# Kernel optimization log

Measured on AMD Instinct MI355X. Metric: run time of the kernel, lower is better.

The kernel has to match this reference:

```python
import jax, jax.numpy as jnp
import numpy as np

N_EXPERTS = 64
TOP_K = 4
D_MODEL = 512
D_FF = 2048
B, T = 2, 1024


def setup_inputs() -> dict:
    key = jax.random.key(0)
    k1, k2, k3, k4 = jax.random.split(key, 4)
    x = jax.random.normal(k1, (B, T, D_MODEL), dtype=jnp.float32)
    hex_weights = jax.random.uniform(k2, (B, T, N_EXPERTS), dtype=jnp.float32)
    W_in = jax.random.normal(k3, (N_EXPERTS, D_FF, D_MODEL), dtype=jnp.float32) * (D_MODEL ** -0.5)
    W_out = jax.random.normal(k4, (N_EXPERTS, D_MODEL, D_FF), dtype=jnp.float32) * (D_FF ** -0.5)
    bias_in = jnp.zeros((N_EXPERTS, D_FF), dtype=jnp.float32)
    bias_out = jnp.zeros((N_EXPERTS, D_MODEL), dtype=jnp.float32)
    return {"x": x, "hex_weights": hex_weights, "W_in": W_in, "bias_in": bias_in,
            "W_out": W_out, "bias_out": bias_out}


def reference(x, hex_weights, W_in, bias_in, W_out, bias_out):
    # x: (B,T,D); hex_weights: (B,T,64)
    Bv, Tv, D = x.shape
    N = Bv * Tv
    xf = x.reshape(N, D)
    hw = hex_weights.reshape(N, N_EXPERTS)
    top_w, top_idx = jax.lax.top_k(hw, TOP_K)                 # (N,K)
    top_w = top_w / (jnp.sum(top_w, axis=-1, keepdims=True) + 1e-8)
    # Sparse combine matrix: row n has top_w at selected experts, 0 elsewhere.
    combine = jnp.zeros((N, N_EXPERTS), dtype=x.dtype).at[
        jnp.arange(N)[:, None], top_idx].add(top_w)            # (N,64)
    # Scan over the 64 experts; equivalent math to per-token weight gather,
    # since combine is zero for unselected experts.
    def body(acc, ew):
        Wi, bi, Wo, bo, c = ew                                 # Wi:(d_ff,D), c:(N,)
        h = jax.nn.silu(xf @ Wi.T + bi)                        # (N,d_ff)
        o = h @ Wo.T + bo                                      # (N,D)
        return acc + c[:, None] * o, None
    out, _ = jax.lax.scan(body, jnp.zeros_like(xf),
                          (W_in, bias_in, W_out, bias_out, combine.T))
    return out.reshape(Bv, Tv, D)
```

## Files before the change

kernel.cpp:

```cpp
#include <hip/hip_runtime.h>
#include <hip/hip_bf16.h>
#include <stdint.h>

#define NTOK 2048
#define NE 64
#define TOPK 4
#define DM 512
#define DF 2048
#define TOTSLOT (NTOK*TOPK)

#define BM 192
#define BK 64
#define GEMM_GRID 1024

typedef __bf16 bf16;
typedef __bf16 bf16x8 __attribute__((ext_vector_type(8)));
typedef __bf16 bf16x4 __attribute__((ext_vector_type(4)));
typedef float  f32x4  __attribute__((ext_vector_type(4)));
typedef short  short8 __attribute__((ext_vector_type(8)));


__global__ void k_route(const float* __restrict__ hw, float* __restrict__ top_w,
                        int* __restrict__ top_idx) {
  int t = blockIdx.x * blockDim.x + threadIdx.x;
  if (t >= NTOK) return;
  const float* r = hw + (size_t)t * NE;
  float rv[NE];
  #pragma unroll
  for (int e = 0; e < NE; ++e) rv[e] = r[e];
  float v[TOPK]; int id[TOPK];
  #pragma unroll
  for (int k = 0; k < TOPK; ++k) {
    float best = -1e30f; int bi = 0;
    #pragma unroll
    for (int e = 0; e < NE; ++e) {
      bool used = false;
      #pragma unroll
      for (int j = 0; j < k; ++j) used |= (id[j] == e);
      if (!used && rv[e] > best) { best = rv[e]; bi = e; }
    }
    v[k] = best; id[k] = bi;
  }
  float den = v[0] + v[1] + v[2] + v[3] + 1e-8f;
  #pragma unroll
  for (int k = 0; k < TOPK; ++k) {
    top_w[t*TOPK + k] = v[k] / den;
    top_idx[t*TOPK + k] = id[k];
  }
}

__global__ __launch_bounds__(256) void k_build(
    const int* __restrict__ top_idx, int* __restrict__ tok,
    int* __restrict__ slot_of, int* __restrict__ offsets_g,
    int* __restrict__ tasklist, int* __restrict__ ntask_g) {
  __shared__ int cnt_s[NE], off_s[NE + 1], fill_s[NE], tpre_s[NE + 1];
  const int tid = threadIdx.x;
  if (tid < NE) { cnt_s[tid] = 0; fill_s[tid] = 0; }
  __syncthreads();
  int ids[TOTSLOT / 256];
  #pragma unroll
  for (int c = 0; c < TOTSLOT / 256; ++c) {
    ids[c] = top_idx[c * 256 + tid];
    atomicAdd(&cnt_s[ids[c]], 1);
  }
  __syncthreads();
  if (tid < 64) {
    int c = cnt_s[tid];
    int inc = c;
    #pragma unroll
    for (int d = 1; d < 64; d <<= 1) {
      int n = __shfl_up(inc, d, 64);
      if (tid >= d) inc += n;
    }
    off_s[tid] = inc - c;
    if (tid == 63) off_s[64] = inc;

    int tc = (c + BM - 1) / BM;
    int tinc = tc;
    #pragma unroll
    for (int d = 1; d < 64; d <<= 1) {
      int n = __shfl_up(tinc, d, 64);
      if (tid >= d) tinc += n;
    }
    tpre_s[tid] = tinc - tc;
    if (tid == 63) tpre_s[64] = tinc;
  }
  __syncthreads();
  #pragma unroll
  for (int c = 0; c < TOTSLOT / 256; ++c) {
    int idx = c * 256 + tid;
    int e = ids[c];
    int pos = off_s[e] + atomicAdd(&fill_s[e], 1);
    tok[pos] = idx >> 2;
    slot_of[idx] = pos;
  }
  if (tid < 64) {
    int tc = (cnt_s[tid] + BM - 1) / BM;
    int base = tpre_s[tid];
    for (int m = 0; m < tc; ++m) tasklist[base + m] = (tid << 8) | m;
    if (tid == 0) *ntask_g = tpre_s[64];
  }
  if (tid <= NE) offsets_g[tid] = off_s[tid];
}

__global__ void k_xcast(const float* __restrict__ x, bf16* __restrict__ xb) {
  int i = blockIdx.x * blockDim.x + threadIdx.x;
  int base = i * 4;
  if (base >= NTOK * DM) return;
  float4 f = *(const float4*)(x + base);
  bf16x4 o;
  o[0] = (bf16)f.x; o[1] = (bf16)f.y; o[2] = (bf16)f.z; o[3] = (bf16)f.w;
  *(bf16x4*)(xb + base) = o;
}


template<int PASS, int BNT>
__global__ __launch_bounds__(512) void k_gemm(
    const float* __restrict__ W, const float* __restrict__ bias,
    const bf16* __restrict__ Asrc, const int* __restrict__ tok,
    const int* __restrict__ offsets,
    const int* __restrict__ tasklist, const int* __restrict__ ntask_g,
    bf16* __restrict__ Hout, float* __restrict__ Oout)
{
  constexpr int KFULL = (PASS == 1) ? DM : DF;
  constexpr int KT    = KFULL / BK;
  constexpr int NDIM  = (PASS == 1) ? DF : DM;
  constexpr int NT    = NDIM / BNT;
  constexpr int TPR   = 512 / BNT;
  constexpr int NQ    = 16 / TPR;
  constexpr int NJ    = BNT / 32;

  const int tid = threadIdx.x;
  const int wave = tid >> 6, lane = tid & 63;
  const int wm = wave >> 1, wn = wave & 1;
  const int lrow = lane >> 4, lcol = lane & 15;

  __shared__ bf16 As[BM * BK];
  __shared__ bf16 Bs[BNT * BK];

  const int ntask = *ntask_g;
  const int gPerXcd = (ntask + 7) / 8;
  const int tot = 8 * gPerXcd * NT;

  #pragma unroll 1
  for (int tt = blockIdx.x; tt < tot; tt += GEMM_GRID) {
    const int xcd  = tt & 7;
    const int v    = tt >> 3;
    const int gloc = v / NT;
    const int ntile= v % NT;
    const int g    = xcd * gPerXcd + gloc;
    if (g >= ntask) continue;
    const int em = tasklist[g];
    const int e  = em >> 8;
    const int mt = em & 255;

    const int off = offsets[e];
    const int cnt = offsets[e+1] - off;
    const int rowcount = cnt - mt * BM;

    const bf16* abase[3]; bool aok[3];
    #pragma unroll
    for (int c = 0; c < 3; ++c) {
      int r = (c * 512 + tid) >> 3;
      aok[c] = (r < rowcount);
      int srcrow;
      if (PASS == 1) srcrow = aok[c] ? tok[off + mt*BM + r] : 0;
      else           srcrow = min(off + mt*BM + (aok[c] ? r : 0), TOTSLOT - 1);
      abase[c] = Asrc + (size_t)srcrow * KFULL + (tid & 7) * 8;
    }
    const int brow = tid / TPR;
    const int bseg = tid % TPR;
    const float* bbase = W + (size_t)e * NDIM * KFULL
                           + (size_t)(ntile*BNT + brow) * KFULL + bseg * (NQ*4);

    f32x4 acc[3][NJ];
    #pragma unroll
    for (int i = 0; i < 3; ++i)
      #pragma unroll
      for (int j = 0; j < NJ; ++j) acc[i][j] = (f32x4)(0.0f);

    #pragma unroll 1
    for (int kt = 0; kt < KT; ++kt) {
      const int k0 = kt * BK;
      short8 areg[3];
      #pragma unroll
      for (int c = 0; c < 3; ++c) {
        if (PASS == 2 || aok[c]) areg[c] = *(const short8*)(abase[c] + k0);
        else                     areg[c] = (short8){0,0,0,0,0,0,0,0};
      }
      float4 breg[NQ];
      #pragma unroll
      for (int q = 0; q < NQ; ++q) breg[q] = *(const float4*)(bbase + k0 + q*4);

      __syncthreads();
      #pragma unroll
      for (int c = 0; c < 3; ++c) {
        int r = (c * 512 + tid) >> 3;
        int u = tid & 7;
        *(short8*)(&As[r*BK + ((u ^ (r & 7)) * 8)]) = areg[c];
      }
      #pragma unroll
      for (int q = 0; q < NQ; ++q) {
        bf16x4 p;
        p[0] = (bf16)breg[q].x; p[1] = (bf16)breg[q].y;
        p[2] = (bf16)breg[q].z; p[3] = (bf16)breg[q].w;
        int s = bseg * NQ + q;
        int unit = s >> 1, half = s & 1;
        *(bf16x4*)((char*)&Bs[0] + brow*128 + ((unit ^ (brow & 7)) * 16) + half*8) = p;
      }
      __syncthreads();

      #pragma unroll
      for (int ksub = 0; ksub < 2; ++ksub) {
        const int uu = ksub*4 + lrow;
        bf16x8 af[3], bfr[NJ];
        #pragma unroll
        for (int i = 0; i < 3; ++i) {
          int m = wm*48 + i*16 + lcol;
          af[i] = *(const bf16x8*)(&As[m*BK + ((uu ^ (m & 7)) * 8)]);
        }
        #pragma unroll
        for (int j = 0; j < NJ; ++j) {
          int n = wn*(BNT/2) + j*16 + lcol;
          bfr[j] = *(const bf16x8*)(&Bs[n*BK + ((uu ^ (n & 7)) * 8)]);
        }
        #pragma unroll
        for (int i = 0; i < 3; ++i)
          #pragma unroll
          for (int j = 0; j < NJ; ++j)
            acc[i][j] = __builtin_amdgcn_mfma_f32_16x16x32_bf16(af[i], bfr[j], acc[i][j], 0, 0, 0);
      }
    }

    const int slotbase = off + mt * BM;
    #pragma unroll
    for (int i = 0; i < 3; ++i) {
      const int rbase = wm*48 + i*16 + lrow*4;
      #pragma unroll
      for (int j = 0; j < NJ; ++j) {
        const int gcol = ntile*BNT + wn*(BNT/2) + j*16 + lcol;
        const float bv = bias[(size_t)e * NDIM + gcol];
        #pragma unroll
        for (int q = 0; q < 4; ++q) {
          const int r = rbase + q;
          if (r < rowcount) {
            float h = acc[i][j][q] + bv;
            if (PASS == 1) {
              float s = h / (1.0f + __expf(-h));
              Hout[(size_t)(slotbase + r) * DF + gcol] = (bf16)s;
            } else {
              Oout[(size_t)(slotbase + r) * DM + gcol] = h;
            }
          }
        }
      }
    }
    __syncthreads();
  }
}


__global__ void k_combine(const float* __restrict__ O, const float* __restrict__ top_w,
                          const int* __restrict__ slot_of, float* __restrict__ out) {
  int i = blockIdx.x * blockDim.x + threadIdx.x;
  if (i >= NTOK * DM / 4) return;
  int t  = i / (DM / 4);
  int d4 = (i % (DM / 4)) * 4;
  float4 s = {0.f, 0.f, 0.f, 0.f};
  #pragma unroll
  for (int k = 0; k < TOPK; ++k) {
    float w = top_w[t*TOPK + k];
    int  sl = slot_of[t*TOPK + k];
    float4 o = *(const float4*)(O + (size_t)sl * DM + d4);
    s.x += w * o.x; s.y += w * o.y; s.z += w * o.z; s.w += w * o.w;
  }
  *(float4*)(out + (size_t)t * DM + d4) = s;
}


extern "C" void kernel_launch(void* const* d_in, const int* in_sizes, int n_in,
                              void* d_out, int out_size, void* d_ws, size_t ws_size,
                              hipStream_t stream) {
  const float* x        = (const float*)d_in[0];
  const float* hw       = (const float*)d_in[1];
  const float* W_in     = (const float*)d_in[2];
  const float* bias_in  = (const float*)d_in[3];
  const float* W_out    = (const float*)d_in[4];
  const float* bias_out = (const float*)d_in[5];
  float* out = (float*)d_out;

  char* ws = (char*)d_ws;
  int*   offsets  = (int*)  (ws + 0);
  int*   ntask    = (int*)  (ws + 512);
  int*   tasklist = (int*)  (ws + 768);
  int*   top_idx  = (int*)  (ws + 2048);
  float* top_w    = (float*)(ws + 2048 + 32768);
  int*   slot_of  = (int*)  (ws + 2048 + 2*32768);
  int*   tok      = (int*)  (ws + 2048 + 3*32768);
  bf16*  xb       = (bf16*) (ws + 2048 + 4*32768);
  size_t o_xb_end = 2048 + 4*32768 + (size_t)NTOK*DM*2;
  bf16*  H        = (bf16*) (ws + o_xb_end);
  size_t o_H_end  = o_xb_end + (size_t)TOTSLOT*DF*2;
  float* O        = (float*)(ws + o_H_end);

  k_route<<<NTOK/256, 256, 0, stream>>>(hw, top_w, top_idx);
  k_build<<<1, 256, 0, stream>>>(top_idx, tok, slot_of, offsets, tasklist, ntask);
  k_xcast<<<(NTOK*DM/4)/256, 256, 0, stream>>>(x, xb);

  k_gemm<1,128><<<GEMM_GRID, 512, 0, stream>>>(W_in, bias_in, xb, tok, offsets,
                                               tasklist, ntask, H, nullptr);
  k_gemm<2,32><<<GEMM_GRID, 512, 0, stream>>>(W_out, bias_out, H, nullptr, offsets,
                                              tasklist, ntask, nullptr, O);

  k_combine<<<(NTOK*DM/4)/256, 256, 0, stream>>>(O, top_w, slot_of, out);
}
```

Baseline: 209.2 us.

## Double-buffer GEMM tiles via direct global-to-LDS loads, keep B fp32 in LDS

The grouped expert GEMM now stages A and B tiles straight from global memory into LDS with global_load_lds, double-buffered so the next k-tile loads while the current one computes. B weights are kept as fp32 in LDS with an XOR swizzle and converted to bf16 at fragment-read time instead of before the LDS store. Pass 1 drops its N tile from 128 to 64 to fit the larger fp32 LDS footprint. This removes the register round-trip and one barrier per iteration, but doubles LDS traffic for B, adds conversion work inside the MFMA loop and lowers per-block reuse in pass 1.

```diff
diff --git a/kernel.cpp b/kernel.cpp
--- a/kernel.cpp
+++ b/kernel.cpp
@@ -17,7 +17,10 @@
 typedef __bf16 bf16x8 __attribute__((ext_vector_type(8)));
 typedef __bf16 bf16x4 __attribute__((ext_vector_type(4)));
 typedef float  f32x4  __attribute__((ext_vector_type(4)));
-typedef short  short8 __attribute__((ext_vector_type(8)));
+
+#define GLD_LDS16(g, l) __builtin_amdgcn_global_load_lds( \
+    (const __attribute__((address_space(1))) void*)(g),   \
+    (__attribute__((address_space(3))) void*)(l), 16, 0, 0)
 
 
 __global__ void k_route(const float* __restrict__ hw, float* __restrict__ top_w,
@@ -126,17 +129,16 @@
   constexpr int KT    = KFULL / BK;
   constexpr int NDIM  = (PASS == 1) ? DF : DM;
   constexpr int NT    = NDIM / BNT;
-  constexpr int TPR   = 512 / BNT;
-  constexpr int NQ    = 16 / TPR;
   constexpr int NJ    = BNT / 32;
+  constexpr int BCH   = (BNT * BK * 4) / (512*16);
 
   const int tid = threadIdx.x;
-  const int wave = tid >> 6, lane = tid & 63;
-  const int wm = wave >> 1, wn = wave & 1;
+  const int w = tid >> 6, lane = tid & 63;
+  const int wm = w >> 1, wn = w & 1;
   const int lrow = lane >> 4, lcol = lane & 15;
 
-  __shared__ bf16 As[BM * BK];
-  __shared__ bf16 Bs[BNT * BK];
+  __shared__ bf16  As[2][BM * BK];
+  __shared__ float Bsf[2][BNT * BK];
 
   const int ntask = *ntask_g;
   const int gPerXcd = (ntask + 7) / 8;
@@ -158,20 +160,33 @@
     const int cnt = offsets[e+1] - off;
     const int rowcount = cnt - mt * BM;
 
-    const bf16* abase[3]; bool aok[3];
+    const bf16* aptr[3];
     #pragma unroll
     for (int c = 0; c < 3; ++c) {
-      int r = (c * 512 + tid) >> 3;
-      aok[c] = (r < rowcount);
-      int srcrow;
-      if (PASS == 1) srcrow = aok[c] ? tok[off + mt*BM + r] : 0;
-      else           srcrow = min(off + mt*BM + (aok[c] ? r : 0), TOTSLOT - 1);
-      abase[c] = Asrc + (size_t)srcrow * KFULL + (tid & 7) * 8;
-    }
-    const int brow = tid / TPR;
-    const int bseg = tid % TPR;
-    const float* bbase = W + (size_t)e * NDIM * KFULL
-                           + (size_t)(ntile*BNT + brow) * KFULL + bseg * (NQ*4);
+      int i = c * 512 + tid;
+      int r = i >> 3, u = tid & 7;
+      int rr = min(r, rowcount - 1);
+      int srcrow = (PASS == 1) ? tok[off + mt*BM + rr]
+                               : min(off + mt*BM + rr, TOTSLOT - 1);
+      aptr[c] = Asrc + (size_t)srcrow * KFULL + ((u ^ (r & 7)) * 8);
+    }
+    const float* bptr[BCH];
+    #pragma unroll
+    for (int s = 0; s < BCH; ++s) {
+      int i = s * 512 + tid;
+      int row = i >> 4, u = tid & 15;
+      bptr[s] = W + (size_t)e * NDIM * KFULL + (size_t)(ntile*BNT + row) * KFULL
+                  + ((u ^ (row & 15)) * 4);
+    }
+
+    auto STAGE = [&](int kt, int b) {
+      #pragma unroll
+      for (int c = 0; c < 3; ++c)
+        GLD_LDS16(aptr[c] + kt*BK, (char*)&As[b][0] + c*8192 + w*1024);
+      #pragma unroll
+      for (int s = 0; s < BCH; ++s)
+        GLD_LDS16(bptr[s] + kt*BK, (char*)&Bsf[b][0] + s*8192 + w*1024);
+    };
 
     f32x4 acc[3][NJ];
     #pragma unroll
@@ -179,50 +194,23 @@
       #pragma unroll
       for (int j = 0; j < NJ; ++j) acc[i][j] = (f32x4)(0.0f);
 
-    #pragma unroll 1
-    for (int kt = 0; kt < KT; ++kt) {
-      const int k0 = kt * BK;
-      short8 areg[3];
-      #pragma unroll
-      for (int c = 0; c < 3; ++c) {
-        if (PASS == 2 || aok[c]) areg[c] = *(const short8*)(abase[c] + k0);
-        else                     areg[c] = (short8){0,0,0,0,0,0,0,0};
-      }
-      float4 breg[NQ];
-      #pragma unroll
-      for (int q = 0; q < NQ; ++q) breg[q] = *(const float4*)(bbase + k0 + q*4);
-
-      __syncthreads();
-      #pragma unroll
-      for (int c = 0; c < 3; ++c) {
-        int r = (c * 512 + tid) >> 3;
-        int u = tid & 7;
-        *(short8*)(&As[r*BK + ((u ^ (r & 7)) * 8)]) = areg[c];
-      }
-      #pragma unroll
-      for (int q = 0; q < NQ; ++q) {
-        bf16x4 p;
-        p[0] = (bf16)breg[q].x; p[1] = (bf16)breg[q].y;
-        p[2] = (bf16)breg[q].z; p[3] = (bf16)breg[q].w;
-        int s = bseg * NQ + q;
-        int unit = s >> 1, half = s & 1;
-        *(bf16x4*)((char*)&Bs[0] + brow*128 + ((unit ^ (brow & 7)) * 16) + half*8) = p;
-      }
-      __syncthreads();
-
-      #pragma unroll
-      for (int ksub = 0; ksub < 2; ++ksub) {
-        const int uu = ksub*4 + lrow;
+    auto COMPUTE = [&](int b) {
+      #pragma unroll
+      for (int ks = 0; ks < 2; ++ks) {
+        const int uu = ks*4 + lrow;
         bf16x8 af[3], bfr[NJ];
         #pragma unroll
         for (int i = 0; i < 3; ++i) {
           int m = wm*48 + i*16 + lcol;
-          af[i] = *(const bf16x8*)(&As[m*BK + ((uu ^ (m & 7)) * 8)]);
+          af[i] = *(const bf16x8*)(&As[b][m*BK + ((uu ^ (m & 7)) * 8)]);
         }
         #pragma unroll
         for (int j = 0; j < NJ; ++j) {
           int n = wn*(BNT/2) + j*16 + lcol;
-          bfr[j] = *(const bf16x8*)(&Bs[n*BK + ((uu ^ (n & 7)) * 8)]);
+          float4 fa = *(const float4*)(&Bsf[b][n*BK + (((2*uu  ) ^ (n & 15)) * 4)]);
+          float4 fb = *(const float4*)(&Bsf[b][n*BK + (((2*uu+1) ^ (n & 15)) * 4)]);
+          bfr[j][0]=(bf16)fa.x; bfr[j][1]=(bf16)fa.y; bfr[j][2]=(bf16)fa.z; bfr[j][3]=(bf16)fa.w;
+          bfr[j][4]=(bf16)fb.x; bfr[j][5]=(bf16)fb.y; bfr[j][6]=(bf16)fb.z; bfr[j][7]=(bf16)fb.w;
         }
         #pragma unroll
         for (int i = 0; i < 3; ++i)
@@ -230,6 +218,17 @@
           for (int j = 0; j < NJ; ++j)
             acc[i][j] = __builtin_amdgcn_mfma_f32_16x16x32_bf16(af[i], bfr[j], acc[i][j], 0, 0, 0);
       }
+    };
+
+    STAGE(0, 0);
+    __syncthreads();
+    int cur = 0;
+    #pragma unroll 1
+    for (int kt = 0; kt < KT; ++kt) {
+      if (kt + 1 < KT) STAGE(kt + 1, cur ^ 1);
+      COMPUTE(cur);
+      __syncthreads();
+      cur ^= 1;
     }
 
     const int slotbase = off + mt * BM;
@@ -255,7 +254,6 @@
         }
       }
     }
-    __syncthreads();
   }
 }
 
@@ -307,8 +305,8 @@
   k_build<<<1, 256, 0, stream>>>(top_idx, tok, slot_of, offsets, tasklist, ntask);
   k_xcast<<<(NTOK*DM/4)/256, 256, 0, stream>>>(x, xb);
 
-  k_gemm<1,128><<<GEMM_GRID, 512, 0, stream>>>(W_in, bias_in, xb, tok, offsets,
-                                               tasklist, ntask, H, nullptr);
+  k_gemm<1,64><<<GEMM_GRID, 512, 0, stream>>>(W_in, bias_in, xb, tok, offsets,
+                                              tasklist, ntask, H, nullptr);
   k_gemm<2,32><<<GEMM_GRID, 512, 0, stream>>>(W_out, bias_out, H, nullptr, offsets,
                                               tasklist, ntask, nullptr, O);
 
```

Result: no change. 212.1 us (+1.4%).
